# Kernel optimization log

Measured on AMD Instinct MI355X. Metric: run time of the kernel, lower is better.

The kernel has to match this reference:

```python
import jax, jax.numpy as jnp
import numpy as np
from jax import lax

B, N = 2048, 8192


def setup_inputs() -> dict:
    key = jax.random.key(0)
    k1, k2 = jax.random.split(key)
    # alpha in [0, 0.3) keeps the tridiagonal system diagonally dominant in fp32
    alpha = 0.3 * jax.random.uniform(k1, (B, N), dtype=jnp.float32)
    f = jax.random.normal(k2, (N,), dtype=jnp.float32)
    return {"alpha": alpha, "f": f}


def _thomas(a, b, c, f):
    """Batched Thomas solve. a: (B,N-1) sub, b: (B,N) diag, c: (B,N-1) super, f: (B,N)."""
    Bn = b.shape[0]
    a_p = jnp.pad(a, ((0, 0), (1, 0)))  # a_0 := 0
    c_p = jnp.pad(c, ((0, 0), (0, 1)))  # c_{N-1} := 0

    def fwd(carry, x):
        cp_prev, dp_prev = carry
        ai, bi, ci, fi = x
        denom = bi - ai * cp_prev
        cp = ci / denom
        dp = (fi - ai * dp_prev) / denom
        return (cp, dp), (cp, dp)

    zeros = jnp.zeros((Bn,), dtype=b.dtype)
    _, (cps, dps) = lax.scan(fwd, (zeros, zeros), (a_p.T, b.T, c_p.T, f.T))

    def bwd(u_next, x):
        cp, dp = x
        u = dp - cp * u_next
        return u, u

    _, us = lax.scan(bwd, zeros, (cps, dps), reverse=True)
    return us.T  # (B, N)


def reference(alpha, f):
    # Tridiagonal matrix A(alpha)
    a = alpha[:, :-1] ** 2                      # subdiagonal
    b = 1.0 + alpha ** 3                        # diagonal
    c = alpha[:, 1:] ** 2 + 2.0 * alpha[:, 1:]  # superdiagonal
    f_b = jnp.broadcast_to(f, alpha.shape)      # (B, N)
    return _thomas(a, b, c, f_b)
```

## Files before the change

kernel.cpp:

```cpp
#include <hip/hip_runtime.h>


#define NN 8192
#define TB 1024
#define CH 8
#define NWAVE (TB/64)

__device__ __forceinline__ float frcp(float x) { return __builtin_amdgcn_rcpf(x); }

#define COMPOSE(p2,q2,r2,s2,t2,u2,v2, p1,q1,r1,s1,t1,u1,v1, P,Q,R,S,T,U,V) \
    { P = (p2)*(p1) + (q2)*(u1);                                           \
      Q = (p2)*(q1) + (q2)*(v1);                                           \
      R = (r2)*(p1) + (s2)*(r1) + (t2)*(u1);                               \
      S = (s2)*(s1);                                                       \
      T = (r2)*(q1) + (s2)*(t1) + (t2)*(v1);                               \
      U = (u2)*(p1) + (v2)*(u1);                                           \
      V = (u2)*(q1) + (v2)*(v1); }

__global__ __launch_bounds__(TB, 8)
void thomas_scan_kernel(const float* __restrict__ alpha,
                        const float* __restrict__ fvec,
                        float* __restrict__ out)
{
    __shared__ float wtot[NWAVE][7];
    __shared__ float btot[NWAVE][2];

    const int t    = threadIdx.x;
    const int lane = t & 63;
    const int wid  = t >> 6;
    const int row  = blockIdx.x;
    const float* __restrict__ arow = alpha + (size_t)row * NN;
    const int base = t * CH;

    float va[CH], vf[CH];
    {
        const float4* a4 = reinterpret_cast<const float4*>(arow + base);
        const float4* f4 = reinterpret_cast<const float4*>(fvec + base);
        #pragma unroll
        for (int k = 0; k < CH / 4; ++k) {
            float4 x = a4[k];
            va[4*k+0]=x.x; va[4*k+1]=x.y; va[4*k+2]=x.z; va[4*k+3]=x.w;
            float4 y = f4[k];
            vf[4*k+0]=y.x; vf[4*k+1]=y.y; vf[4*k+2]=y.z; vf[4*k+3]=y.w;
        }
    }
    const float aL = (t > 0)      ? arow[base - 1]  : 0.0f;
    const float aR = (t < TB - 1) ? arow[base + CH] : 0.0f;

    float p=1.f, q=0.f, r=0.f, s=1.f, tt=0.f, u=0.f, v=1.f;
    #pragma unroll
    for (int k = 0; k < CH; ++k) {
        const float am1 = (k == 0)      ? aL : va[k-1];
        const float ap1 = (k == CH - 1) ? aR : va[k+1];
        const float ai = am1 * am1;
        const float bi = 1.0f + va[k]*va[k]*va[k];
        const float ci = ap1 * (ap1 + 2.0f);
        const float fi = vf[k];
        const float np = ci*u,        nq = ci*v;
        const float nr = fi*u - ai*r, ns = -ai*s, nt = fi*v - ai*tt;
        const float nu = bi*u - ai*p, nv = bi*v - ai*q;
        p=np; q=nq; r=nr; s=ns; tt=nt; u=nu; v=nv;
    }
    { const float inv = frcp(v); p*=inv; q*=inv; r*=inv; s*=inv; tt*=inv; u*=inv; v=1.0f; }

    #pragma unroll
    for (int off = 1; off < 64; off <<= 1) {
        const float p1 = __shfl_up(p, off);
        const float q1 = __shfl_up(q, off);
        const float r1 = __shfl_up(r, off);
        const float s1 = __shfl_up(s, off);
        const float t1 = __shfl_up(tt, off);
        const float u1 = __shfl_up(u, off);
        const float v1 = __shfl_up(v, off);
        if (lane >= off) {
            float np,nq,nr,ns,nt,nu,nv;
            COMPOSE(p,q,r,s,tt,u,v, p1,q1,r1,s1,t1,u1,v1, np,nq,nr,ns,nt,nu,nv);
            p=np; q=nq; r=nr; s=ns; tt=nt; u=nu; v=nv;
        }
    }
    if (lane == 63) {
        wtot[wid][0]=p; wtot[wid][1]=q; wtot[wid][2]=r; wtot[wid][3]=s;
        wtot[wid][4]=tt; wtot[wid][5]=u; wtot[wid][6]=v;
    }
    __syncthreads();

    float ep=__shfl_up(p,1), eq=__shfl_up(q,1), er=__shfl_up(r,1),
          es=__shfl_up(s,1), et=__shfl_up(tt,1), eu=__shfl_up(u,1), ev=__shfl_up(v,1);
    if (lane == 0) { ep=1.f; eq=0.f; er=0.f; es=1.f; et=0.f; eu=0.f; ev=1.f; }

    float Pp=1.f, Pq=0.f, Pr=0.f, Ps=1.f, Pt=0.f, Pu=0.f, Pv=1.f;
    for (int w = 0; w < wid; ++w) {
        const float p1=wtot[w][0], q1=wtot[w][1], r1=wtot[w][2], s1=wtot[w][3],
                    t1=wtot[w][4], u1=wtot[w][5], v1=wtot[w][6];
        float np,nq,nr,ns,nt,nu,nv;
        COMPOSE(p1,q1,r1,s1,t1,u1,v1, Pp,Pq,Pr,Ps,Pt,Pu,Pv, np,nq,nr,ns,nt,nu,nv);
        Pp=np; Pq=nq; Pr=nr; Ps=ns; Pt=nt; Pu=nu; Pv=nv;
    }
    float cp, dp;
    {
        const float nq = ep*Pq + eq*Pv;
        const float nt = er*Pq + es*Pt + et*Pv;
        const float nv = eu*Pq + ev*Pv;
        const float inv = frcp(nv);
        cp = nq*inv; dp = nt*inv;
    }

    float cpv[CH], dpv[CH];
    #pragma unroll
    for (int k = 0; k < CH; ++k) {
        const float am1 = (k == 0)      ? aL : va[k-1];
        const float ap1 = (k == CH - 1) ? aR : va[k+1];
        const float ai = am1 * am1;
        const float bi = 1.0f + va[k]*va[k]*va[k];
        const float ci = ap1 * (ap1 + 2.0f);
        const float rd = frcp(bi - ai*cp);
        cp = ci * rd;
        dp = (vf[k] - ai*dp) * rd;
        cpv[k] = cp; dpv[k] = dp;
    }

    float A = 1.0f, Bb = 0.0f;
    #pragma unroll
    for (int k = CH - 1; k >= 0; --k) {
        Bb = dpv[k] - cpv[k]*Bb;
        A  = -cpv[k]*A;
    }
    #pragma unroll
    for (int off = 1; off < 64; off <<= 1) {
        const float A1 = __shfl_down(A, off);
        const float B1 = __shfl_down(Bb, off);
        if (lane < 64 - off) { Bb = A*B1 + Bb; A = A*A1; }
    }
    if (lane == 0) { btot[wid][0] = A; btot[wid][1] = Bb; }
    __syncthreads();

    float eA = __shfl_down(A, 1), eB = __shfl_down(Bb, 1);
    if (lane == 63) { eA = 1.0f; eB = 0.0f; }
    float SA = 1.0f, SB = 0.0f;
    for (int w = NWAVE - 1; w > wid; --w) {
        const float A1 = btot[w][0], B1 = btot[w][1];
        SB = A1*SB + B1;
        SA = A1*SA;
    }
    const float u_in = eA*SB + eB;

    float uv[CH];
    float un = u_in;
    #pragma unroll
    for (int k = CH - 1; k >= 0; --k) {
        un = dpv[k] - cpv[k]*un;
        uv[k] = un;
    }
    float4* o4 = reinterpret_cast<float4*>(out + (size_t)row * NN + base);
    #pragma unroll
    for (int k = 0; k < CH / 4; ++k) {
        o4[k] = make_float4(uv[4*k+0], uv[4*k+1], uv[4*k+2], uv[4*k+3]);
    }
}

extern "C" void kernel_launch(void* const* d_in, const int* in_sizes, int n_in,
                              void* d_out, int out_size, void* d_ws, size_t ws_size,
                              hipStream_t stream) {
    const float* alpha = (const float*)d_in[0];
    const float* fvec  = (const float*)d_in[1];
    float* out = (float*)d_out;
    const int nrows = out_size / NN;
    thomas_scan_kernel<<<nrows, TB, 0, stream>>>(alpha, fvec, out);
}
```

Baseline: 130.2 us.

## Split forward scan into 2x2 Möbius scan plus separate affine dp scan

After: 150.5 us. 15.6% more time.

```diff
diff --git a/kernel.cpp b/kernel.cpp
--- a/kernel.cpp
+++ b/kernel.cpp
@@ -8,22 +8,14 @@
 
 __device__ __forceinline__ float frcp(float x) { return __builtin_amdgcn_rcpf(x); }
 
-#define COMPOSE(p2,q2,r2,s2,t2,u2,v2, p1,q1,r1,s1,t1,u1,v1, P,Q,R,S,T,U,V) \
-    { P = (p2)*(p1) + (q2)*(u1);                                           \
-      Q = (p2)*(q1) + (q2)*(v1);                                           \
-      R = (r2)*(p1) + (s2)*(r1) + (t2)*(u1);                               \
-      S = (s2)*(s1);                                                       \
-      T = (r2)*(q1) + (s2)*(t1) + (t2)*(v1);                               \
-      U = (u2)*(p1) + (v2)*(u1);                                           \
-      V = (u2)*(q1) + (v2)*(v1); }
-
 __global__ __launch_bounds__(TB, 8)
 void thomas_scan_kernel(const float* __restrict__ alpha,
                         const float* __restrict__ fvec,
                         float* __restrict__ out)
 {
-    __shared__ float wtot[NWAVE][7];
-    __shared__ float btot[NWAVE][2];
+    __shared__ __align__(16) float wtot[NWAVE][4];
+    __shared__ __align__(8)  float dtot[NWAVE][2];
+    __shared__ __align__(8)  float btot[NWAVE][2];
 
     const int t    = threadIdx.x;
     const int lane = t & 63;
@@ -47,7 +39,7 @@
     const float aL = (t > 0)      ? arow[base - 1]  : 0.0f;
     const float aR = (t < TB - 1) ? arow[base + CH] : 0.0f;
 
-    float p=1.f, q=0.f, r=0.f, s=1.f, tt=0.f, u=0.f, v=1.f;
+    float p=1.f, q=0.f, u=0.f, v=1.f;
     #pragma unroll
     for (int k = 0; k < CH; ++k) {
         const float am1 = (k == 0)      ? aL : va[k-1];
@@ -55,69 +47,86 @@
         const float ai = am1 * am1;
         const float bi = 1.0f + va[k]*va[k]*va[k];
         const float ci = ap1 * (ap1 + 2.0f);
-        const float fi = vf[k];
         const float np = ci*u,        nq = ci*v;
-        const float nr = fi*u - ai*r, ns = -ai*s, nt = fi*v - ai*tt;
         const float nu = bi*u - ai*p, nv = bi*v - ai*q;
-        p=np; q=nq; r=nr; s=ns; tt=nt; u=nu; v=nv;
+        p=np; q=nq; u=nu; v=nv;
     }
-    { const float inv = frcp(v); p*=inv; q*=inv; r*=inv; s*=inv; tt*=inv; u*=inv; v=1.0f; }
+    { const float inv = frcp(v); p*=inv; q*=inv; u*=inv; v=1.0f; }
 
     #pragma unroll
     for (int off = 1; off < 64; off <<= 1) {
-        const float p1 = __shfl_up(p, off);
-        const float q1 = __shfl_up(q, off);
-        const float r1 = __shfl_up(r, off);
-        const float s1 = __shfl_up(s, off);
-        const float t1 = __shfl_up(tt, off);
-        const float u1 = __shfl_up(u, off);
-        const float v1 = __shfl_up(v, off);
+        const float p1=__shfl_up(p,off), q1=__shfl_up(q,off),
+                    u1=__shfl_up(u,off), v1=__shfl_up(v,off);
         if (lane >= off) {
-            float np,nq,nr,ns,nt,nu,nv;
-            COMPOSE(p,q,r,s,tt,u,v, p1,q1,r1,s1,t1,u1,v1, np,nq,nr,ns,nt,nu,nv);
-            p=np; q=nq; r=nr; s=ns; tt=nt; u=nu; v=nv;
+            const float np = p*p1 + q*u1, nq = p*q1 + q*v1;
+            const float nu = u*p1 + v*u1, nv = u*q1 + v*v1;
+            p=np; q=nq; u=nu; v=nv;
         }
     }
-    if (lane == 63) {
-        wtot[wid][0]=p; wtot[wid][1]=q; wtot[wid][2]=r; wtot[wid][3]=s;
-        wtot[wid][4]=tt; wtot[wid][5]=u; wtot[wid][6]=v;
-    }
+    if (lane == 63) { wtot[wid][0]=p; wtot[wid][1]=q; wtot[wid][2]=u; wtot[wid][3]=v; }
     __syncthreads();
 
-    float ep=__shfl_up(p,1), eq=__shfl_up(q,1), er=__shfl_up(r,1),
-          es=__shfl_up(s,1), et=__shfl_up(tt,1), eu=__shfl_up(u,1), ev=__shfl_up(v,1);
-    if (lane == 0) { ep=1.f; eq=0.f; er=0.f; es=1.f; et=0.f; eu=0.f; ev=1.f; }
+    float ep=__shfl_up(p,1), eq=__shfl_up(q,1), eu=__shfl_up(u,1), ev=__shfl_up(v,1);
+    if (lane == 0) { ep=1.f; eq=0.f; eu=0.f; ev=1.f; }
 
-    float Pp=1.f, Pq=0.f, Pr=0.f, Ps=1.f, Pt=0.f, Pu=0.f, Pv=1.f;
+    float Pq = 0.f, Pv = 1.f;
     for (int w = 0; w < wid; ++w) {
-        const float p1=wtot[w][0], q1=wtot[w][1], r1=wtot[w][2], s1=wtot[w][3],
-                    t1=wtot[w][4], u1=wtot[w][5], v1=wtot[w][6];
-        float np,nq,nr,ns,nt,nu,nv;
-        COMPOSE(p1,q1,r1,s1,t1,u1,v1, Pp,Pq,Pr,Ps,Pt,Pu,Pv, np,nq,nr,ns,nt,nu,nv);
-        Pp=np; Pq=nq; Pr=nr; Ps=ns; Pt=nt; Pu=nu; Pv=nv;
+        const float4 T = *reinterpret_cast<const float4*>(wtot[w]);
+        const float nq = T.x*Pq + T.y*Pv;
+        const float nv = T.z*Pq + T.w*Pv;
+        Pq = nq; Pv = nv;
     }
-    float cp, dp;
+    float cp;
     {
-        const float nq = ep*Pq + eq*Pv;
-        const float nt = er*Pq + es*Pt + et*Pv;
-        const float nv = eu*Pq + ev*Pv;
-        const float inv = frcp(nv);
-        cp = nq*inv; dp = nt*inv;
+        const float nx = ep*Pq + eq*Pv;
+        const float nz = eu*Pq + ev*Pv;
+        cp = nx * frcp(nz);
     }
 
-    float cpv[CH], dpv[CH];
+    float cpv[CH], asv[CH], bsv[CH];
+    {
+        float xp = cp, zp = 1.0f, yb = 0.0f, al = 1.0f;
+        #pragma unroll
+        for (int k = 0; k < CH; ++k) {
+            const float am1 = (k == 0)      ? aL : va[k-1];
+            const float ap1 = (k == CH - 1) ? aR : va[k+1];
+            const float ai = am1 * am1;
+            const float bi = 1.0f + va[k]*va[k]*va[k];
+            const float ci = ap1 * (ap1 + 2.0f);
+            const float x = ci * zp;
+            const float z = bi*zp - ai*xp;
+            const float y = vf[k]*zp - ai*yb;
+            al = -ai * al;
+            const float rdz = frcp(z);
+            cpv[k] = x  * rdz;
+            asv[k] = al * rdz;
+            bsv[k] = y  * rdz;
+            xp = x; zp = z; yb = y;
+        }
+    }
+
+    float Ad = asv[CH-1], Bd = bsv[CH-1];
     #pragma unroll
-    for (int k = 0; k < CH; ++k) {
-        const float am1 = (k == 0)      ? aL : va[k-1];
-        const float ap1 = (k == CH - 1) ? aR : va[k+1];
-        const float ai = am1 * am1;
-        const float bi = 1.0f + va[k]*va[k]*va[k];
-        const float ci = ap1 * (ap1 + 2.0f);
-        const float rd = frcp(bi - ai*cp);
-        cp = ci * rd;
-        dp = (vf[k] - ai*dp) * rd;
-        cpv[k] = cp; dpv[k] = dp;
+    for (int off = 1; off < 64; off <<= 1) {
+        const float A1 = __shfl_up(Ad, off);
+        const float B1 = __shfl_up(Bd, off);
+        if (lane >= off) { Bd = Ad*B1 + Bd; Ad = Ad*A1; }
     }
+    if (lane == 63) { dtot[wid][0]=Ad; dtot[wid][1]=Bd; }
+    __syncthreads();
+
+    float eAd = __shfl_up(Ad,1), eBd = __shfl_up(Bd,1);
+    if (lane == 0) { eAd = 1.0f; eBd = 0.0f; }
+    float PB = 0.f;
+    for (int w = 0; w < wid; ++w) {
+        const float2 T = *reinterpret_cast<const float2*>(dtot[w]);
+        PB = T.x*PB + T.y;
+    }
+    const float dp_in = eAd*PB + eBd;
+
+    float dpv[CH];
+    #pragma unroll
+    for (int k = 0; k < CH; ++k) dpv[k] = bsv[k] + dp_in*asv[k];
 
     float A = 1.0f, Bb = 0.0f;
     #pragma unroll
@@ -136,11 +145,10 @@
 
     float eA = __shfl_down(A, 1), eB = __shfl_down(Bb, 1);
     if (lane == 63) { eA = 1.0f; eB = 0.0f; }
-    float SA = 1.0f, SB = 0.0f;
+    float SB = 0.f;
     for (int w = NWAVE - 1; w > wid; --w) {
-        const float A1 = btot[w][0], B1 = btot[w][1];
-        SB = A1*SB + B1;
-        SA = A1*SA;
+        const float2 T = *reinterpret_cast<const float2*>(btot[w]);
+        SB = T.x*SB + T.y;
     }
     const float u_in = eA*SB + eB;
 
```
